# Kernel tuning notes

Measured on AMD Instinct MI355X. Metric: run time of the kernel, lower is better.

The kernel has to match this reference:

```python
import jax, jax.numpy as jnp
import numpy as np
import math

C = jnp.complex64
PI = math.pi
N = 4
D = 2 ** N  # 16

# ---- static single/two-qubit building blocks (numpy, complex64) ----
_I2 = np.eye(2, dtype=np.complex64)
_H = np.array([[1, 1], [1, -1]], dtype=np.complex64) / math.sqrt(2)

def _kron_list(ms):
    out = ms[0]
    for m in ms[1:]:
        out = np.kron(out, m)
    return out

# Hadamard expanded to qubit i of 4 (qubit 0 = most significant)
_HGATES = [jnp.asarray(_kron_list([_I2] * i + [_H] + [_I2] * (N - 1 - i))) for i in range(N)]

def _swap(i, j):
    idx = np.arange(D)
    bi = (idx >> (N - 1 - i)) & 1
    bj = (idx >> (N - 1 - j)) & 1
    d = bi ^ bj
    sw = idx ^ ((d << (N - 1 - i)) | (d << (N - 1 - j)))
    P = np.zeros((D, D), dtype=np.complex64)
    P[sw, idx] = 1.0
    return jnp.asarray(P)

_SW03 = _swap(0, 3)
_SW12 = _swap(1, 2)

# projectors on qubits 0,1 (4x4): |00><00|, |11><11|, |+><+|, |-><-| (Bell-like pair states)
_s0 = np.array([1, 0], dtype=np.complex64)
_s1 = np.array([0, 1], dtype=np.complex64)
_s00 = np.kron(_s0, _s0); _s11 = np.kron(_s1, _s1)
_sp = (np.kron(_s0, _s1) + np.kron(_s1, _s0)) / math.sqrt(2)
_sm = (np.kron(_s0, _s1) - np.kron(_s1, _s0)) / math.sqrt(2)
_P00 = jnp.asarray(np.outer(_s00, _s00.conj()))
_P11 = jnp.asarray(np.outer(_s11, _s11.conj()))
_Ppp = jnp.asarray(np.outer(_sp, _sp.conj()))
_Pmm = jnp.asarray(np.outer(_sm, _sm.conj()))
# Um = I4, so its term is a constant 16x16 matrix
_KMM = jnp.asarray(np.kron(np.outer(_sm, _sm.conj()), np.eye(4, dtype=np.complex64)))


def _blk(e, c0, c3):
    # [[c0,0,0,0],[0,a,b,0],[0,b,a,0],[0,0,0,c3]] with a=(e+1)/2, b=(e-1)/2
    one = jnp.ones((), C)
    z = jnp.zeros((), C)
    a = (e + one) * 0.5
    b = (e - one) * 0.5
    return jnp.stack([
        jnp.stack([c0, z, z, z]),
        jnp.stack([z, a, b, z]),
        jnp.stack([z, b, a, z]),
        jnp.stack([z, z, z, c3]),
    ])


def _U16(t):
    # t: float scalar. ep = e^{it}, em = e^{-it}
    ep = jax.lax.complex(jnp.cos(t), jnp.sin(t)).astype(C)
    em = jnp.conj(ep)
    one = jnp.ones((), C)
    U00 = _blk(em, one, em)
    U11 = _blk(ep, ep, one)
    z = jnp.zeros((), C)
    Up = jnp.diag(jnp.stack([ep, one, one, em]))
    return (jnp.kron(_P00, U00) + jnp.kron(_P11, U11)
            + jnp.kron(_Ppp, Up) + _KMM)


def _qft_U(thetas):
    oper = jnp.eye(D, dtype=C)
    n = 0
    for i in range(N):
        oper = _HGATES[i] @ oper
        for _ in range(i + 1, N):
            oper = _U16(thetas[n]) @ oper
            n += 1
    oper = _SW03 @ oper
    oper = _SW12 @ oper
    return oper


def setup_inputs() -> dict:
    key = jax.random.key(0)
    k1, k2, k3 = jax.random.split(key, 3)
    B, M = 8192, 128
    return {
        "inputs_re": jax.random.normal(k1, (B, D, M), dtype=jnp.float32),
        "inputs_im": jax.random.normal(k2, (B, D, M), dtype=jnp.float32),
        "thetas": jax.random.uniform(k3, (6,), dtype=jnp.float32, minval=0.0, maxval=2 * PI),
    }


def reference(inputs_re, inputs_im, thetas):
    inp = jax.lax.complex(inputs_re, inputs_im)  # [B,16,M] complex64
    gate = _qft_U(thetas)                        # [16,16] complex64
    # tf.matmul(qft_U, inputs) broadcast over batch
    return jnp.einsum("ij,bjm->bim", gate, inp)
```

## Files before the change

kernel.cpp:

```cpp
#include <hip/hip_runtime.h>

__device__ inline unsigned int f2bf(float f) {
    unsigned int u = __float_as_uint(f);
    u += 0x7fffu + ((u >> 16) & 1u);
    return u >> 16;
}

__device__ inline void u16_row(int r, float2 ep, int* c0, float2* v0, int* c1, float2* v1) {
    float2 em   = make_float2(ep.x, -ep.y);
    float2 one  = make_float2(1.f, 0.f);
    float2 zero = make_float2(0.f, 0.f);
    int pr = r >> 2, qr = r & 3;
    if (pr == 0 || pr == 3) {
        float2 e   = (pr == 0) ? em  : ep;
        float2 cc0 = (pr == 0) ? one : ep;
        float2 cc3 = (pr == 0) ? em  : one;
        int base = (pr == 0) ? 0 : 12;
        float2 a = make_float2((e.x + 1.f) * .5f, e.y * .5f);
        float2 b = make_float2((e.x - 1.f) * .5f, e.y * .5f);
        if      (qr == 0) { *c0 = base + 0; *v0 = cc0; *c1 = base + 0; *v1 = zero; }
        else if (qr == 3) { *c0 = base + 3; *v0 = cc3; *c1 = base + 3; *v1 = zero; }
        else if (qr == 1) { *c0 = base + 1; *v0 = a;   *c1 = base + 2; *v1 = b;    }
        else              { *c0 = base + 1; *v0 = b;   *c1 = base + 2; *v1 = a;    }
    } else {
        float2 up = (qr == 0) ? ep : (qr == 3 ? em : one);
        float hx = up.x * .5f, hy = up.y * .5f;
        float s1 = (pr == 1) ? 0.5f : -0.5f;
        float s2 = (pr == 2) ? 0.5f : -0.5f;
        *c0 = 4 + qr; *v0 = make_float2(hx + s1, hy);
        *c1 = 8 + qr; *v1 = make_float2(hx + s2, hy);
    }
}

__global__ __launch_bounds__(256, 4) void qft_fused_kernel(
    const float* __restrict__ re, const float* __restrict__ im,
    const float* __restrict__ thetas, unsigned short* __restrict__ out)
{
    __shared__ float2 A[2][16][16];
    int tid  = threadIdx.x;
    int b    = blockIdx.x * 4 + (tid >> 6);
    int lane = tid & 63;
    int gi = tid >> 4, gj = tid & 15;

    const float2* pr = reinterpret_cast<const float2*>(re + b * 2048) + lane;
    const float2* pi = reinterpret_cast<const float2*>(im + b * 2048) + lane;
    float2 xr[16], xi[16];
#pragma unroll
    for (int j = 0; j < 16; ++j) { xr[j] = pr[j * 64]; xi[j] = pi[j * 64]; }

    A[0][gi][gj] = make_float2((gi == gj) ? 1.f : 0.f, 0.f);
    __syncthreads();
    const signed char kind [10] = {-1, 0, 0, 0, -1, 0, 0, -1, 0, -1};
    const signed char param[10] = { 0, 0, 1, 2,  1, 3, 4,  2, 5,  3};
#pragma unroll
    for (int s = 0; s < 10; ++s) {
        int src = s & 1, dst = src ^ 1;
        float2 acc;
        if (kind[s] < 0) {
            int p  = 3 - param[s];
            int i0 = gi & ~(1 << p), i1 = gi | (1 << p);
            const float rt = 0.70710678118654752f;
            float sg = ((gi >> p) & 1) ? -rt : rt;
            float2 a0 = A[src][i0][gj], a1 = A[src][i1][gj];
            acc.x = rt * a0.x + sg * a1.x;
            acc.y = rt * a0.y + sg * a1.y;
        } else {
            float th = thetas[(int)param[s]];
            float2 ep = make_float2(cosf(th), -sinf(th));
            int c0, c1; float2 v0, v1;
            u16_row(gi, ep, &c0, &v0, &c1, &v1);
            float2 a0 = A[src][c0][gj], a1 = A[src][c1][gj];
            acc.x = v0.x * a0.x - v0.y * a0.y + v1.x * a1.x - v1.y * a1.y;
            acc.y = v0.x * a0.y + v0.y * a0.x + v1.x * a1.y + v1.y * a1.x;
        }
        A[dst][gi][gj] = acc;
        __syncthreads();
    }

    unsigned short* po = out + (size_t)b * 4096 + lane * 4;
#pragma unroll
    for (int i = 0; i < 16; ++i) {
        const int rr = ((i & 1) << 3) | ((i & 2) << 1) | ((i & 4) >> 1) | ((i & 8) >> 3);
        float ar0 = 0.f, ai0 = 0.f, ar1 = 0.f, ai1 = 0.f;
#pragma unroll
        for (int j = 0; j < 16; ++j) {
            float2 g = A[0][rr][j];
            ar0 = fmaf(g.x, xr[j].x, ar0); ar0 = fmaf(-g.y, xi[j].x, ar0);
            ai0 = fmaf(g.y, xr[j].x, ai0); ai0 = fmaf(g.x, xi[j].x, ai0);
            ar1 = fmaf(g.x, xr[j].y, ar1); ar1 = fmaf(-g.y, xi[j].y, ar1);
            ai1 = fmaf(g.y, xr[j].y, ai1); ai1 = fmaf(g.x, xi[j].y, ai1);
        }
        uint2 w;
        w.x = f2bf(ar0) | (f2bf(ai0) << 16);
        w.y = f2bf(ar1) | (f2bf(ai1) << 16);
        *reinterpret_cast<uint2*>(po + (size_t)i * 256) = w;
    }
}

extern "C" void kernel_launch(void* const* d_in, const int* in_sizes, int n_in,
                              void* d_out, int out_size, void* d_ws, size_t ws_size,
                              hipStream_t stream) {
    const float* im = (const float*)d_in[0];
    const float* re = (const float*)d_in[1];
    const float* th = (const float*)d_in[2];
    unsigned short* out = (unsigned short*)d_out;

    int B = in_sizes[0] / (16 * 128);
    qft_fused_kernel<<<B / 4, 256, 0, stream>>>(re, im, th, out);
}
```

Measured before the change: 181.9 us.

## Remap threads to one column per thread with streamed input and transposed gate

Each thread now owns one column instead of two, so each block covers two batches and the grid doubles. The gate matrix is transposed in shared memory with the output row permutation folded in, which allows input to be streamed column-by-column into 16 complex accumulators instead of holding 32 float2 registers of input. Input loads are no longer issued before the gate build, so that latency is not overlapped with the gate computation. Each block now computes the gate for only two batches, doubling the redundant gate-build work, and output stores shrink to 4-byte writes.

```diff
diff --git a/kernel.cpp b/kernel.cpp
--- a/kernel.cpp
+++ b/kernel.cpp
@@ -37,16 +37,8 @@
     const float* __restrict__ thetas, unsigned short* __restrict__ out)
 {
     __shared__ float2 A[2][16][16];
-    int tid  = threadIdx.x;
-    int b    = blockIdx.x * 4 + (tid >> 6);
-    int lane = tid & 63;
+    int tid = threadIdx.x;
     int gi = tid >> 4, gj = tid & 15;
-
-    const float2* pr = reinterpret_cast<const float2*>(re + b * 2048) + lane;
-    const float2* pi = reinterpret_cast<const float2*>(im + b * 2048) + lane;
-    float2 xr[16], xi[16];
-#pragma unroll
-    for (int j = 0; j < 16; ++j) { xr[j] = pr[j * 64]; xi[j] = pi[j * 64]; }
 
     A[0][gi][gj] = make_float2((gi == gj) ? 1.f : 0.f, 0.f);
     __syncthreads();
@@ -76,24 +68,39 @@
         A[dst][gi][gj] = acc;
         __syncthreads();
     }
+    {
+        int rg = ((gj & 1) << 3) | ((gj & 2) << 1) | ((gj & 4) >> 1) | ((gj & 8) >> 3);
+        float2 v = A[0][rg][gi];
+        __syncthreads();
+        A[1][gi][gj] = v;
+        __syncthreads();
+    }
 
-    unsigned short* po = out + (size_t)b * 4096 + lane * 4;
+    int b   = blockIdx.x * 2 + (tid >> 7);
+    int col = tid & 127;
+    const float* prr = re + b * 2048 + col;
+    const float* pri = im + b * 2048 + col;
+
+    float ar[16], ai[16];
+#pragma unroll
+    for (int i = 0; i < 16; ++i) { ar[i] = 0.f; ai[i] = 0.f; }
+
+#pragma unroll
+    for (int j = 0; j < 16; ++j) {
+        float xr = prr[j * 128];
+        float xi = pri[j * 128];
+#pragma unroll
+        for (int i = 0; i < 16; ++i) {
+            float2 g = A[1][j][i];
+            ar[i] = fmaf(g.x, xr, ar[i]); ar[i] = fmaf(-g.y, xi, ar[i]);
+            ai[i] = fmaf(g.y, xr, ai[i]); ai[i] = fmaf(g.x, xi, ai[i]);
+        }
+    }
+
+    unsigned short* po = out + (size_t)b * 4096 + col * 2;
 #pragma unroll
     for (int i = 0; i < 16; ++i) {
-        const int rr = ((i & 1) << 3) | ((i & 2) << 1) | ((i & 4) >> 1) | ((i & 8) >> 3);
-        float ar0 = 0.f, ai0 = 0.f, ar1 = 0.f, ai1 = 0.f;
-#pragma unroll
-        for (int j = 0; j < 16; ++j) {
-            float2 g = A[0][rr][j];
-            ar0 = fmaf(g.x, xr[j].x, ar0); ar0 = fmaf(-g.y, xi[j].x, ar0);
-            ai0 = fmaf(g.y, xr[j].x, ai0); ai0 = fmaf(g.x, xi[j].x, ai0);
-            ar1 = fmaf(g.x, xr[j].y, ar1); ar1 = fmaf(-g.y, xi[j].y, ar1);
-            ai1 = fmaf(g.y, xr[j].y, ai1); ai1 = fmaf(g.x, xi[j].y, ai1);
-        }
-        uint2 w;
-        w.x = f2bf(ar0) | (f2bf(ai0) << 16);
-        w.y = f2bf(ar1) | (f2bf(ai1) << 16);
-        *reinterpret_cast<uint2*>(po + (size_t)i * 256) = w;
+        *reinterpret_cast<unsigned int*>(po + (size_t)i * 256) = f2bf(ar[i]) | (f2bf(ai[i]) << 16);
     }
 }
 
@@ -106,5 +113,5 @@
     unsigned short* out = (unsigned short*)d_out;
 
     int B = in_sizes[0] / (16 * 128);
-    qft_fused_kernel<<<B / 4, 256, 0, stream>>>(re, im, th, out);
+    qft_fused_kernel<<<B / 2, 256, 0, stream>>>(re, im, th, out);
 }
```

After: 179.7 us. About the same (-1.2%).
